# Kernel optimization log

Measured on AMD Instinct MI355X. Metric: run time of the kernel, lower is better.

Reference implementation:

```python
import jax, jax.numpy as jnp
import numpy as np

N, E, D, L = 50000, 640000, 128, 3  # nodes, edges, channels, layers
EPS = 1e-5


def setup_inputs() -> dict:
    key = jax.random.key(0)
    ks = jax.random.split(key, 10)
    s = 1.0 / np.sqrt(D)
    inp = {
        "x": jax.random.normal(ks[0], (N, D), dtype=jnp.float32),
        "edge_attr": jax.random.normal(ks[1], (E, D), dtype=jnp.float32),
        "w_self": jax.random.normal(ks[2], (L, D, D), dtype=jnp.float32) * s,
        "b_self": jnp.zeros((L, D), dtype=jnp.float32),
        "w_in": jax.random.normal(ks[3], (L, D, D), dtype=jnp.float32) * s,
        "b_in": jnp.zeros((L, D), dtype=jnp.float32),
        "w_rel": jax.random.normal(ks[4], (L, D, D), dtype=jnp.float32) * s,
        "b_rel": jnp.zeros((L, D), dtype=jnp.float32),
        "bn_gamma": jnp.ones((L - 1, D), dtype=jnp.float32),
        "bn_beta": jnp.zeros((L - 1, D), dtype=jnp.float32),
        "edge_index": jax.random.randint(ks[5], (2, E), 0, N, dtype=jnp.int64),
    }
    return inp


def _batchnorm(h, gamma, beta):
    mu = jnp.mean(h, axis=0)
    var = jnp.mean(jnp.square(h - mu), axis=0)  # biased var (torch BN training)
    return (h - mu) * jax.lax.rsqrt(var + EPS) * gamma + beta


def reference(x, edge_attr, w_self, b_self, w_in, b_in, w_rel, b_rel,
              bn_gamma, bn_beta, edge_index):
    src, dst = edge_index[0], edge_index[1]
    # per-node in-degree for mean aggregation (zero-degree nodes -> 0)
    cnt = jax.ops.segment_sum(jnp.ones((E, 1), x.dtype), dst, num_segments=N)
    denom = jnp.maximum(cnt, 1.0)
    for i in range(L):
        # message: lin_in(x_j * edge_attr)
        msg = jnp.einsum('ed,fd->ef', x[src] * edge_attr, w_in[i]) + b_in[i]
        agg = jax.ops.segment_sum(msg, dst, num_segments=N) / denom  # scatter-mean
        x = agg + jnp.einsum('nd,fd->nf', x, w_self[i]) + b_self[i]
        edge_attr = jnp.einsum('ed,fd->ef', edge_attr, w_rel[i]) + b_rel[i]
        if i < L - 1:
            x = jax.nn.relu(_batchnorm(x, bn_gamma[i], bn_beta[i]))
            # dropout p=0.0 -> identity
    return (x, edge_attr)
```

## Files before the change

### kernel.cpp

```cpp
#include <hip/hip_runtime.h>

#define DD 128

typedef __attribute__((ext_vector_type(8))) short bf16x8;
typedef __attribute__((ext_vector_type(4))) short bf16x4;
typedef __attribute__((ext_vector_type(4))) float f32x4;
typedef unsigned short u16;

__device__ __forceinline__ unsigned short f2bf(float f) {
  union { float f; unsigned u; } v; v.f = f;
  unsigned u = v.u;
  return (unsigned short)((u + 0x7FFFu + ((u >> 16) & 1u)) >> 16);
}
__device__ __forceinline__ float bf2f(unsigned short h) {
  union { unsigned u; float f; } v; v.u = ((unsigned)h) << 16; return v.f;
}

__device__ __forceinline__ bf16x8 pack8(f32x4 a, f32x4 b) {
  bf16x8 r;
  r[0] = (short)f2bf(a.x); r[1] = (short)f2bf(a.y);
  r[2] = (short)f2bf(a.z); r[3] = (short)f2bf(a.w);
  r[4] = (short)f2bf(b.x); r[5] = (short)f2bf(b.y);
  r[6] = (short)f2bf(b.z); r[7] = (short)f2bf(b.w);
  return r;
}

__device__ __forceinline__ bool idx_is64(const int* p) {
  return (p[1] | p[3] | p[5] | p[7]) == 0;
}
__device__ __forceinline__ int ld_idx(const int* p, long long i, bool is64) {
  return is64 ? (int)((const long long*)p)[i] : p[i];
}

__global__ void k_count(const int* __restrict__ idx, int* __restrict__ cnt, int E) {
  int e = blockIdx.x * blockDim.x + threadIdx.x;
  if (e >= E) return;
  bool is64 = idx_is64(idx);
  int d = ld_idx(idx, (long long)E + e, is64);
  atomicAdd(&cnt[d], 1);
}

__global__ __launch_bounds__(1024) void k_scan(const int* __restrict__ cnt,
    int* __restrict__ row_start, int* __restrict__ cursor, int N) {
  __shared__ int part[1024];
  int t = threadIdx.x;
  int chunk = (N + 1023) >> 10;
  int lo = t * chunk, hi = lo + chunk; if (hi > N) hi = N; if (lo > N) lo = N;
  int s = 0;
  for (int i = lo; i < hi; ++i) s += cnt[i];
  part[t] = s;
  __syncthreads();
  for (int off = 1; off < 1024; off <<= 1) {
    int v = (t >= off) ? part[t - off] : 0;
    __syncthreads();
    part[t] += v;
    __syncthreads();
  }
  int run = (t == 0) ? 0 : part[t - 1];
  for (int i = lo; i < hi; ++i) {
    row_start[i] = run; cursor[i] = run; run += cnt[i];
  }
  if (t == 1023) row_start[N] = part[1023];
}

__global__ void k_fill(const int* __restrict__ idx, int* __restrict__ cursor,
                       int* __restrict__ edge_of, int* __restrict__ src_csr, int E) {
  int e = blockIdx.x * blockDim.x + threadIdx.x;
  if (e >= E) return;
  bool is64 = idx_is64(idx);
  int s = ld_idx(idx, e, is64);
  int d = ld_idx(idx, (long long)E + e, is64);
  int pos = atomicAdd(&cursor[d], 1);
  edge_of[pos] = e;
  src_csr[pos] = s;
}

__global__ __launch_bounds__(256) void k_agg0(const float* __restrict__ x,
    const float* __restrict__ ea, const int* __restrict__ edge_of,
    const int* __restrict__ src_csr, const int* __restrict__ row_start,
    float* __restrict__ aggm, u16* __restrict__ eaC) {
  int n = blockIdx.x * 4 + (threadIdx.x >> 6);
  int lane = threadIdx.x & 63;
  int esub = lane >> 4, cg = lane & 15;
  int c0 = cg * 8;
  int s0 = row_start[n], s1 = row_start[n + 1];
  int len = s1 - s0;
  float acc[8];
#pragma unroll
  for (int j = 0; j < 8; ++j) acc[j] = 0.f;
  for (int kk = 0; kk < len; kk += 4) {
    int kx = kk + esub;
    bool act = kx < len;
    int k = s0 + (act ? kx : 0);
    int e = edge_of[k];
    int sn = src_csr[k];
    f32x4 e0 = *(const f32x4*)(ea + (size_t)e * DD + c0);
    f32x4 e1 = *(const f32x4*)(ea + (size_t)e * DD + c0 + 4);
    f32x4 x0 = *(const f32x4*)(x + (size_t)sn * DD + c0);
    f32x4 x1 = *(const f32x4*)(x + (size_t)sn * DD + c0 + 4);
    if (act) {
      *(bf16x8*)(eaC + (size_t)k * DD + c0) = pack8(e0, e1);
#pragma unroll
      for (int j = 0; j < 4; ++j) acc[j] += x0[j] * e0[j];
#pragma unroll
      for (int j = 0; j < 4; ++j) acc[4 + j] += x1[j] * e1[j];
    }
  }
  float inv = (len > 0) ? 1.0f / (float)len : 0.0f;
#pragma unroll
  for (int j = 0; j < 8; ++j) {
    float s = acc[j];
    s += __shfl_xor(s, 16);
    s += __shfl_xor(s, 32);
    acc[j] = s * inv;
  }
  if (esub == 0) {
    f32x4 lo, hi;
#pragma unroll
    for (int j = 0; j < 4; ++j) { lo[j] = acc[j]; hi[j] = acc[4 + j]; }
    *(f32x4*)(aggm + (size_t)n * DD + c0) = lo;
    *(f32x4*)(aggm + (size_t)n * DD + c0 + 4) = hi;
  }
}

__global__ __launch_bounds__(256) void k_aggN(const u16* __restrict__ xb,
    const u16* __restrict__ eaC, const int* __restrict__ src_csr,
    const int* __restrict__ row_start, const float* __restrict__ scale,
    const float* __restrict__ shift, float* __restrict__ aggm) {
  int n = blockIdx.x * 4 + (threadIdx.x >> 6);
  int lane = threadIdx.x & 63;
  int esub = lane >> 4, cg = lane & 15;
  int c0 = cg * 8;
  float sc[8], sh[8];
#pragma unroll
  for (int j = 0; j < 8; ++j) { sc[j] = scale[c0 + j]; sh[j] = shift[c0 + j]; }
  int s0 = row_start[n], s1 = row_start[n + 1];
  int len = s1 - s0;
  float acc[8];
#pragma unroll
  for (int j = 0; j < 8; ++j) acc[j] = 0.f;
  for (int kk = 0; kk < len; kk += 4) {
    int kx = kk + esub;
    bool act = kx < len;
    int k = s0 + (act ? kx : 0);
    int sn = src_csr[k];
    bf16x8 ev = *(const bf16x8*)(eaC + (size_t)k * DD + c0);
    bf16x8 xv = *(const bf16x8*)(xb + (size_t)sn * DD + c0);
    if (act) {
#pragma unroll
      for (int j = 0; j < 8; ++j) {
        float xf = fmaxf(bf2f((u16)xv[j]) * sc[j] + sh[j], 0.f);
        acc[j] += xf * bf2f((u16)ev[j]);
      }
    }
  }
  float inv = (len > 0) ? 1.0f / (float)len : 0.0f;
#pragma unroll
  for (int j = 0; j < 8; ++j) {
    float s = acc[j];
    s += __shfl_xor(s, 16);
    s += __shfl_xor(s, 32);
    acc[j] = s * inv;
  }
  if (esub == 0) {
    f32x4 lo, hi;
#pragma unroll
    for (int j = 0; j < 4; ++j) { lo[j] = acc[j]; hi[j] = acc[4 + j]; }
    *(f32x4*)(aggm + (size_t)n * DD + c0) = lo;
    *(f32x4*)(aggm + (size_t)n * DD + c0 + 4) = hi;
  }
}

template <typename TX, bool BN, typename TO, bool STATS>
__global__ __launch_bounds__(256) void k_node(const float* __restrict__ aggm,
    const TX* __restrict__ xc, const float* __restrict__ W_in,
    const float* __restrict__ W_self, const float* __restrict__ b_in,
    const float* __restrict__ b_self, const int* __restrict__ row_start,
    const float* __restrict__ scale, const float* __restrict__ shift,
    TO* __restrict__ xn, float* __restrict__ gsum, float* __restrict__ gssq,
    int ntiles) {
  __shared__ short Wl[DD * 256];
  for (int q = threadIdx.x; q < DD * 256 / 4; q += 256) {
    int off = q * 4;
    int f = off >> 8, k = off & 255;
    f32x4 w = (k < 128) ? *(const f32x4*)(W_in + f * 128 + k)
                        : *(const f32x4*)(W_self + f * 128 + (k - 128));
    unsigned byte = ((unsigned)(f * 512 + k * 2)) ^ (unsigned)((f & 7) << 4);
    bf16x4 s4;
    s4[0] = (short)f2bf(w.x); s4[1] = (short)f2bf(w.y);
    s4[2] = (short)f2bf(w.z); s4[3] = (short)f2bf(w.w);
    *(bf16x4*)((char*)Wl + byte) = s4;
  }
  __syncthreads();
  int wave = threadIdx.x >> 6, lane = threadIdx.x & 63;
  int tile = blockIdx.x * 4 + wave;
  if (tile >= ntiles) return;
  int r = lane & 15, g = lane >> 4;
  int arowi = tile * 16 + r;
  const float* arow = aggm + (size_t)arowi * DD;
  const TX* xrow = xc + (size_t)arowi * DD;
  bf16x8 a[8];
#pragma unroll
  for (int ks = 0; ks < 4; ++ks) {
    const float* p = arow + ks * 32 + g * 8;
    a[ks] = pack8(*(const f32x4*)p, *(const f32x4*)(p + 4));
  }
#pragma unroll
  for (int ks = 0; ks < 4; ++ks) {
    int c0 = ks * 32 + g * 8;
    float v[8];
    if constexpr (sizeof(TX) == 2) {
      bf16x8 raw = *(const bf16x8*)(xrow + c0);
#pragma unroll
      for (int j = 0; j < 8; ++j) v[j] = bf2f((u16)raw[j]);
    } else {
      f32x4 r0 = *(const f32x4*)((const float*)xrow + c0);
      f32x4 r1 = *(const f32x4*)((const float*)xrow + c0 + 4);
#pragma unroll
      for (int j = 0; j < 4; ++j) { v[j] = r0[j]; v[4 + j] = r1[j]; }
    }
    bf16x8 fr;
#pragma unroll
    for (int j = 0; j < 8; ++j) {
      float f = v[j];
      if constexpr (BN) f = fmaxf(f * scale[c0 + j] + shift[c0 + j], 0.f);
      fr[j] = (short)f2bf(f);
    }
    a[4 + ks] = fr;
  }
  f32x4 acc[8];
#pragma unroll
  for (int ct = 0; ct < 8; ++ct) acc[ct] = (f32x4){0.f, 0.f, 0.f, 0.f};
#pragma unroll
  for (int ct = 0; ct < 8; ++ct) {
    int f = ct * 16 + r;
    unsigned base = (unsigned)(f * 512);
    unsigned sw = (unsigned)((f & 7) << 4);
#pragma unroll
    for (int ks = 0; ks < 8; ++ks) {
      unsigned byte = (base + (unsigned)(ks * 64 + g * 16)) ^ sw;
      bf16x8 b = *(const bf16x8*)((const char*)Wl + byte);
      acc[ct] = __builtin_amdgcn_mfma_f32_16x16x32_bf16(a[ks], b, acc[ct], 0, 0, 0);
    }
  }
  int nbase = tile * 16;
  float degmask[4];
#pragma unroll
  for (int j = 0; j < 4; ++j) {
    int nn = nbase + g * 4 + j;
    degmask[j] = (row_start[nn + 1] > row_start[nn]) ? 1.0f : 0.0f;
  }
#pragma unroll
  for (int ct = 0; ct < 8; ++ct) {
    int col = ct * 16 + r;
    float bi = b_in[col], bs = b_self[col];
    float s = 0.f, s2 = 0.f;
#pragma unroll
    for (int j = 0; j < 4; ++j) {
      float v = acc[ct][j] + bs + bi * degmask[j];
      if constexpr (sizeof(TO) == 2) xn[(size_t)(nbase + g * 4 + j) * DD + col] = (TO)f2bf(v);
      else                            xn[(size_t)(nbase + g * 4 + j) * DD + col] = (TO)v;
      s += v; s2 += v * v;
    }
    if constexpr (STATS) {
      s += __shfl_xor(s, 16);  s += __shfl_xor(s, 32);
      s2 += __shfl_xor(s2, 16); s2 += __shfl_xor(s2, 32);
      if (g == 0) { atomicAdd(&gsum[col], s); atomicAdd(&gssq[col], s2); }
    }
  }
}

template <bool SCATTER, typename TO>
__global__ __launch_bounds__(256) void k_rel(const u16* __restrict__ ea_in,
    TO* __restrict__ ea_out, const int* __restrict__ edge_of,
    const float* __restrict__ W, const float* __restrict__ bias, int ntiles) {
  __shared__ short Wl[DD * DD];
  for (int q = threadIdx.x; q < DD * DD / 4; q += 256) {
    int off = q * 4;
    int f = off >> 7, d = off & 127;
    f32x4 w = *(const f32x4*)(W + off);
    unsigned byte = ((unsigned)(f * 256 + d * 2)) ^ (unsigned)((f & 7) << 4);
    bf16x4 s4;
    s4[0] = (short)f2bf(w.x); s4[1] = (short)f2bf(w.y);
    s4[2] = (short)f2bf(w.z); s4[3] = (short)f2bf(w.w);
    *(bf16x4*)((char*)Wl + byte) = s4;
  }
  __syncthreads();
  int wave = threadIdx.x >> 6, lane = threadIdx.x & 63;
  int r = lane & 15, g = lane >> 4;
  for (int tile = blockIdx.x * 4 + wave; tile < ntiles; tile += gridDim.x * 4) {
    const u16* rowp = ea_in + (size_t)(tile * 16 + r) * DD;
    bf16x8 a[4];
#pragma unroll
    for (int ks = 0; ks < 4; ++ks) a[ks] = *(const bf16x8*)(rowp + ks * 32 + g * 8);
    f32x4 acc[8];
#pragma unroll
    for (int ct = 0; ct < 8; ++ct) acc[ct] = (f32x4){0.f, 0.f, 0.f, 0.f};
#pragma unroll
    for (int ct = 0; ct < 8; ++ct) {
      int f = ct * 16 + r;
      unsigned base = (unsigned)(f * 256);
      unsigned sw = (unsigned)((f & 7) << 4);
#pragma unroll
      for (int ks = 0; ks < 4; ++ks) {
        unsigned byte = (base + (unsigned)(ks * 64 + g * 16)) ^ sw;
        bf16x8 b = *(const bf16x8*)((const char*)Wl + byte);
        acc[ct] = __builtin_amdgcn_mfma_f32_16x16x32_bf16(a[ks], b, acc[ct], 0, 0, 0);
      }
    }
    size_t orow[4];
#pragma unroll
    for (int j = 0; j < 4; ++j) {
      int kr = tile * 16 + g * 4 + j;
      orow[j] = SCATTER ? (size_t)edge_of[kr] : (size_t)kr;
    }
#pragma unroll
    for (int ct = 0; ct < 8; ++ct) {
      int col = ct * 16 + r;
      float bv = bias[col];
#pragma unroll
      for (int j = 0; j < 4; ++j) {
        float v = acc[ct][j] + bv;
        if constexpr (sizeof(TO) == 2) ea_out[orow[j] * DD + col] = (TO)f2bf(v);
        else                            ea_out[orow[j] * DD + col] = (TO)v;
      }
    }
  }
}

__global__ void k_bnfin(const float* __restrict__ gsum, const float* __restrict__ gssq,
    const float* __restrict__ gamma, const float* __restrict__ beta,
    float* __restrict__ scale, float* __restrict__ shift, int N) {
  int d = threadIdx.x;
  float mu = gsum[d] / (float)N;
  float var = gssq[d] / (float)N - mu * mu;
  float rs = rsqrtf(var + 1e-5f);
  float sc = rs * gamma[d];
  scale[d] = sc;
  shift[d] = beta[d] - mu * sc;
}

static inline size_t alignup(size_t v, size_t a) { return (v + a - 1) & ~(a - 1); }

extern "C" void kernel_launch(void* const* d_in, const int* in_sizes, int n_in,
                              void* d_out, int out_size, void* d_ws, size_t ws_size,
                              hipStream_t stream) {
  const float* x0     = (const float*)d_in[0];
  const float* ea0    = (const float*)d_in[1];
  const float* w_self = (const float*)d_in[2];
  const float* b_self = (const float*)d_in[3];
  const float* w_in   = (const float*)d_in[4];
  const float* b_in   = (const float*)d_in[5];
  const float* w_rel  = (const float*)d_in[6];
  const float* b_rel  = (const float*)d_in[7];
  const float* gamma  = (const float*)d_in[8];
  const float* beta   = (const float*)d_in[9];
  const int*   idx    = (const int*)d_in[10];

  const int N = in_sizes[0] / DD;
  const int E = in_sizes[1] / DD;

  char* w = (char*)d_ws;
  size_t off = 0;
  int* cnt       = (int*)(w + off); off = alignup(off + (size_t)N * 4, 256);
  int* row_start = (int*)(w + off); off = alignup(off + (size_t)(N + 1) * 4, 256);
  int* cursor    = (int*)(w + off); off = alignup(off + (size_t)N * 4, 256);
  int* edge_of   = (int*)(w + off); off = alignup(off + (size_t)E * 4, 256);
  int* src_csr   = (int*)(w + off); off = alignup(off + (size_t)E * 4, 256);
  float* gstats  = (float*)(w + off); off = alignup(off + 256 * 4, 256);
  float* scale   = (float*)(w + off); off = alignup(off + 128 * 4, 256);
  float* shift   = (float*)(w + off); off = alignup(off + 128 * 4, 256);
  float* aggm    = (float*)(w + off); off = alignup(off + (size_t)N * DD * 4, 256);
  u16*   xb      = (u16*)(w + off);   off = alignup(off + (size_t)N * DD * 2, 256);
  u16*   eaC     = (u16*)(w + off);   off = alignup(off + (size_t)E * DD * 2, 256);
  float* gsum = gstats, *gssq = gstats + 128;
  (void)ws_size; (void)n_in; (void)out_size;

  float* out_x  = (float*)d_out;
  float* out_ea = out_x + (size_t)N * DD;

  (void)hipMemsetAsync(cnt, 0, (size_t)N * 4, stream);
  int ethreads = 256, eblocks = (E + ethreads - 1) / ethreads;
  k_count<<<eblocks, ethreads, 0, stream>>>(idx, cnt, E);
  k_scan<<<1, 1024, 0, stream>>>(cnt, row_start, cursor, N);
  k_fill<<<eblocks, ethreads, 0, stream>>>(idx, cursor, edge_of, src_csr, E);

  const int ntN = N / 16;
  const int ntE = E / 16;
  const int aggBlocks = (N + 3) / 4;
  const int nodeBlocks = (ntN + 3) / 4;
  const int relBlocks = 2048;

  (void)hipMemsetAsync(gstats, 0, 256 * 4, stream);
  k_agg0<<<aggBlocks, 256, 0, stream>>>(x0, ea0, edge_of, src_csr, row_start,
                                        aggm, eaC);
  k_node<float, false, u16, true><<<nodeBlocks, 256, 0, stream>>>(aggm, x0,
      w_in, w_self, b_in, b_self, row_start, scale, shift,
      xb, gsum, gssq, ntN);
  k_rel<false, u16><<<relBlocks, 256, 0, stream>>>(eaC, eaC, edge_of,
      w_rel, b_rel, ntE);
  k_bnfin<<<1, 128, 0, stream>>>(gsum, gssq, gamma, beta, scale, shift, N);

  (void)hipMemsetAsync(gstats, 0, 256 * 4, stream);
  k_aggN<<<aggBlocks, 256, 0, stream>>>(xb, eaC, src_csr, row_start,
                                        scale, shift, aggm);
  k_node<u16, true, u16, true><<<nodeBlocks, 256, 0, stream>>>(aggm, xb,
      w_in + DD * DD, w_self + DD * DD, b_in + DD, b_self + DD,
      row_start, scale, shift, xb, gsum, gssq, ntN);
  k_rel<false, u16><<<relBlocks, 256, 0, stream>>>(eaC, eaC, edge_of,
      w_rel + DD * DD, b_rel + DD, ntE);
  k_bnfin<<<1, 128, 0, stream>>>(gsum, gssq, gamma + DD, beta + DD, scale, shift, N);

  k_aggN<<<aggBlocks, 256, 0, stream>>>(xb, eaC, src_csr, row_start,
                                        scale, shift, aggm);
  k_node<u16, true, float, false><<<nodeBlocks, 256, 0, stream>>>(aggm, xb,
      w_in + 2 * DD * DD, w_self + 2 * DD * DD, b_in + 2 * DD, b_self + 2 * DD,
      row_start, scale, shift, out_x, gsum, gssq, ntN);
  k_rel<true, float><<<relBlocks, 256, 0, stream>>>(eaC, out_ea, edge_of,
      w_rel + 2 * DD * DD, b_rel + 2 * DD, ntE);
}
```

Measured before the change: 1.030 ms.

## Split gather-aggregate into edge-parallel message kernel and CSR segment sum

Replaces the per-node gather-and-accumulate kernels with two steps. An edge-parallel kernel writes per-edge bf16 messages (x_src * edge_attr) to a buffer, and a segmented-sum kernel then reduces them per destination node into a bf16 aggregate. BatchNorm+ReLU moves into a separate apply pass over the node features, and the stats reset is folded into the finalize kernel. k_rel now launches one tile per wave instead of a persistent grid. The aim is better load balance and less uncoalesced gather work, at the cost of writing and re-reading a full E×128 message buffer each layer and extra bf16 rounding of messages and aggregates.

```diff
diff --git a/kernel.cpp b/kernel.cpp
--- a/kernel.cpp
+++ b/kernel.cpp
@@ -15,7 +15,6 @@
 __device__ __forceinline__ float bf2f(unsigned short h) {
   union { unsigned u; float f; } v; v.u = ((unsigned)h) << 16; return v.f;
 }
-
 __device__ __forceinline__ bf16x8 pack8(f32x4 a, f32x4 b) {
   bf16x8 r;
   r[0] = (short)f2bf(a.x); r[1] = (short)f2bf(a.y);
@@ -75,108 +74,132 @@
   src_csr[pos] = s;
 }
 
-__global__ __launch_bounds__(256) void k_agg0(const float* __restrict__ x,
-    const float* __restrict__ ea, const int* __restrict__ edge_of,
-    const int* __restrict__ src_csr, const int* __restrict__ row_start,
-    float* __restrict__ aggm, u16* __restrict__ eaC) {
+template <int MODE>
+__global__ __launch_bounds__(256) void k_msg(
+    const float* __restrict__ x0, const u16* __restrict__ xp,
+    const float* __restrict__ ea0, const u16* __restrict__ eain,
+    u16* __restrict__ m, u16* __restrict__ eaC,
+    const int* __restrict__ edge_of, const int* __restrict__ src_csr, int E) {
+  int i = blockIdx.x * 256 + threadIdx.x;
+  int k = i >> 4, c = i & 15;
+  if (k >= E) return;
+  int sn = src_csr[k];
+  int co = c * 8;
+  bf16x8 mm;
+  if constexpr (MODE == 0) {
+    int e = edge_of[k];
+    const float* ep = ea0 + (size_t)e * DD + co;
+    const float* xq = x0 + (size_t)sn * DD + co;
+    f32x4 e0 = *(const f32x4*)ep, e1 = *(const f32x4*)(ep + 4);
+    f32x4 xv0 = *(const f32x4*)xq, xv1 = *(const f32x4*)(xq + 4);
+    *(bf16x8*)(eaC + (size_t)k * DD + co) = pack8(e0, e1);
+    f32x4 p0 = e0 * xv0, p1 = e1 * xv1;
+    mm = pack8(p0, p1);
+  } else {
+    bf16x8 ev = *(const bf16x8*)(eain + (size_t)k * DD + co);
+    bf16x8 xv = *(const bf16x8*)(xp + (size_t)sn * DD + co);
+#pragma unroll
+    for (int j = 0; j < 8; ++j)
+      mm[j] = (short)f2bf(bf2f((u16)ev[j]) * bf2f((u16)xv[j]));
+  }
+  *(bf16x8*)(m + (size_t)k * DD + co) = mm;
+}
+
+__global__ __launch_bounds__(256) void k_segsum(const u16* __restrict__ m,
+    const int* __restrict__ row_start, u16* __restrict__ agg, int N) {
   int n = blockIdx.x * 4 + (threadIdx.x >> 6);
+  if (n >= N) return;
   int lane = threadIdx.x & 63;
-  int esub = lane >> 4, cg = lane & 15;
-  int c0 = cg * 8;
+  int e4 = lane >> 4, c = lane & 15, co = c * 8;
   int s0 = row_start[n], s1 = row_start[n + 1];
   int len = s1 - s0;
   float acc[8];
 #pragma unroll
   for (int j = 0; j < 8; ++j) acc[j] = 0.f;
-  for (int kk = 0; kk < len; kk += 4) {
-    int kx = kk + esub;
-    bool act = kx < len;
-    int k = s0 + (act ? kx : 0);
-    int e = edge_of[k];
-    int sn = src_csr[k];
-    f32x4 e0 = *(const f32x4*)(ea + (size_t)e * DD + c0);
-    f32x4 e1 = *(const f32x4*)(ea + (size_t)e * DD + c0 + 4);
-    f32x4 x0 = *(const f32x4*)(x + (size_t)sn * DD + c0);
-    f32x4 x1 = *(const f32x4*)(x + (size_t)sn * DD + c0 + 4);
-    if (act) {
-      *(bf16x8*)(eaC + (size_t)k * DD + c0) = pack8(e0, e1);
-#pragma unroll
-      for (int j = 0; j < 4; ++j) acc[j] += x0[j] * e0[j];
-#pragma unroll
-      for (int j = 0; j < 4; ++j) acc[4 + j] += x1[j] * e1[j];
-    }
-  }
-  float inv = (len > 0) ? 1.0f / (float)len : 0.0f;
+  for (int kk = e4; kk < len; kk += 4) {
+    bf16x8 mv = *(const bf16x8*)(m + (size_t)(s0 + kk) * DD + co);
+#pragma unroll
+    for (int j = 0; j < 8; ++j) acc[j] += bf2f((u16)mv[j]);
+  }
 #pragma unroll
   for (int j = 0; j < 8; ++j) {
     float s = acc[j];
     s += __shfl_xor(s, 16);
     s += __shfl_xor(s, 32);
-    acc[j] = s * inv;
-  }
-  if (esub == 0) {
+    acc[j] = s;
+  }
+  if (e4 == 0) {
+    float inv = (len > 0) ? 1.0f / (float)len : 0.0f;
     f32x4 lo, hi;
 #pragma unroll
-    for (int j = 0; j < 4; ++j) { lo[j] = acc[j]; hi[j] = acc[4 + j]; }
-    *(f32x4*)(aggm + (size_t)n * DD + c0) = lo;
-    *(f32x4*)(aggm + (size_t)n * DD + c0 + 4) = hi;
-  }
-}
-
-__global__ __launch_bounds__(256) void k_aggN(const u16* __restrict__ xb,
-    const u16* __restrict__ eaC, const int* __restrict__ src_csr,
-    const int* __restrict__ row_start, const float* __restrict__ scale,
-    const float* __restrict__ shift, float* __restrict__ aggm) {
-  int n = blockIdx.x * 4 + (threadIdx.x >> 6);
-  int lane = threadIdx.x & 63;
-  int esub = lane >> 4, cg = lane & 15;
-  int c0 = cg * 8;
-  float sc[8], sh[8];
-#pragma unroll
-  for (int j = 0; j < 8; ++j) { sc[j] = scale[c0 + j]; sh[j] = shift[c0 + j]; }
-  int s0 = row_start[n], s1 = row_start[n + 1];
-  int len = s1 - s0;
-  float acc[8];
-#pragma unroll
-  for (int j = 0; j < 8; ++j) acc[j] = 0.f;
-  for (int kk = 0; kk < len; kk += 4) {
-    int kx = kk + esub;
-    bool act = kx < len;
-    int k = s0 + (act ? kx : 0);
-    int sn = src_csr[k];
-    bf16x8 ev = *(const bf16x8*)(eaC + (size_t)k * DD + c0);
-    bf16x8 xv = *(const bf16x8*)(xb + (size_t)sn * DD + c0);
-    if (act) {
-#pragma unroll
-      for (int j = 0; j < 8; ++j) {
-        float xf = fmaxf(bf2f((u16)xv[j]) * sc[j] + sh[j], 0.f);
-        acc[j] += xf * bf2f((u16)ev[j]);
-      }
-    }
-  }
-  float inv = (len > 0) ? 1.0f / (float)len : 0.0f;
-#pragma unroll
-  for (int j = 0; j < 8; ++j) {
-    float s = acc[j];
-    s += __shfl_xor(s, 16);
-    s += __shfl_xor(s, 32);
-    acc[j] = s * inv;
-  }
-  if (esub == 0) {
-    f32x4 lo, hi;
-#pragma unroll
-    for (int j = 0; j < 4; ++j) { lo[j] = acc[j]; hi[j] = acc[4 + j]; }
-    *(f32x4*)(aggm + (size_t)n * DD + c0) = lo;
-    *(f32x4*)(aggm + (size_t)n * DD + c0 + 4) = hi;
-  }
-}
-
-template <typename TX, bool BN, typename TO, bool STATS>
-__global__ __launch_bounds__(256) void k_node(const float* __restrict__ aggm,
+    for (int j = 0; j < 4; ++j) { lo[j] = acc[j] * inv; hi[j] = acc[4 + j] * inv; }
+    *(bf16x8*)(agg + (size_t)n * DD + co) = pack8(lo, hi);
+  }
+}
+
+template <bool SCATTER, typename TO>
+__global__ __launch_bounds__(256, 3) void k_rel(const u16* __restrict__ ea_in,
+    TO* __restrict__ ea_out, const int* __restrict__ edge_of,
+    const float* __restrict__ W, const float* __restrict__ bias, int ntiles) {
+  __shared__ short Wl[16384];
+  for (int q = threadIdx.x; q < 4096; q += 256) {
+    int off = q * 4;
+    int f = off >> 7, d = off & 127;
+    f32x4 w = *(const f32x4*)(W + off);
+    unsigned byte = ((unsigned)(f * 256 + d * 2)) ^ (unsigned)((f & 7) << 4);
+    bf16x4 s4;
+    s4[0] = (short)f2bf(w.x); s4[1] = (short)f2bf(w.y);
+    s4[2] = (short)f2bf(w.z); s4[3] = (short)f2bf(w.w);
+    *(bf16x4*)((char*)Wl + byte) = s4;
+  }
+  __syncthreads();
+  int wave = threadIdx.x >> 6, lane = threadIdx.x & 63;
+  int r = lane & 15, g = lane >> 4;
+  int tile = blockIdx.x * 4 + wave;
+  if (tile >= ntiles) return;
+  const u16* rowp = ea_in + (size_t)(tile * 16 + r) * DD;
+  bf16x8 a8[4];
+#pragma unroll
+  for (int ks = 0; ks < 4; ++ks) a8[ks] = *(const bf16x8*)(rowp + ks * 32 + g * 8);
+  f32x4 acc[8];
+#pragma unroll
+  for (int ct = 0; ct < 8; ++ct) acc[ct] = (f32x4){0.f, 0.f, 0.f, 0.f};
+#pragma unroll
+  for (int ct = 0; ct < 8; ++ct) {
+    int f = ct * 16 + r;
+    unsigned base = (unsigned)(f * 256);
+    unsigned sw = (unsigned)((f & 7) << 4);
+#pragma unroll
+    for (int ks = 0; ks < 4; ++ks) {
+      unsigned byte = (base + (unsigned)(ks * 64 + g * 16)) ^ sw;
+      bf16x8 bb = *(const bf16x8*)((const char*)Wl + byte);
+      acc[ct] = __builtin_amdgcn_mfma_f32_16x16x32_bf16(a8[ks], bb, acc[ct], 0, 0, 0);
+    }
+  }
+  size_t orow[4];
+#pragma unroll
+  for (int j = 0; j < 4; ++j) {
+    int kr = tile * 16 + g * 4 + j;
+    orow[j] = SCATTER ? (size_t)edge_of[kr] : (size_t)kr;
+  }
+#pragma unroll
+  for (int ct = 0; ct < 8; ++ct) {
+    int col = ct * 16 + r;
+    float bv = bias[col];
+#pragma unroll
+    for (int j = 0; j < 4; ++j) {
+      float v = acc[ct][j] + bv;
+      if constexpr (sizeof(TO) == 2) ea_out[orow[j] * DD + col] = (TO)f2bf(v);
+      else                            ea_out[orow[j] * DD + col] = (TO)v;
+    }
+  }
+}
+
+template <typename TX, typename TO, bool STATS>
+__global__ __launch_bounds__(256, 2) void k_node(const u16* __restrict__ agg,
     const TX* __restrict__ xc, const float* __restrict__ W_in,
     const float* __restrict__ W_self, const float* __restrict__ b_in,
     const float* __restrict__ b_self, const int* __restrict__ row_start,
-    const float* __restrict__ scale, const float* __restrict__ shift,
     TO* __restrict__ xn, float* __restrict__ gsum, float* __restrict__ gssq,
     int ntiles) {
   __shared__ short Wl[DD * 256];
@@ -197,36 +220,20 @@
   if (tile >= ntiles) return;
   int r = lane & 15, g = lane >> 4;
   int arowi = tile * 16 + r;
-  const float* arow = aggm + (size_t)arowi * DD;
+  const u16* arow = agg + (size_t)arowi * DD;
   const TX* xrow = xc + (size_t)arowi * DD;
   bf16x8 a[8];
 #pragma unroll
-  for (int ks = 0; ks < 4; ++ks) {
-    const float* p = arow + ks * 32 + g * 8;
-    a[ks] = pack8(*(const f32x4*)p, *(const f32x4*)(p + 4));
-  }
+  for (int ks = 0; ks < 4; ++ks) a[ks] = *(const bf16x8*)(arow + ks * 32 + g * 8);
 #pragma unroll
   for (int ks = 0; ks < 4; ++ks) {
     int c0 = ks * 32 + g * 8;
-    float v[8];
     if constexpr (sizeof(TX) == 2) {
-      bf16x8 raw = *(const bf16x8*)(xrow + c0);
-#pragma unroll
-      for (int j = 0; j < 8; ++j) v[j] = bf2f((u16)raw[j]);
+      a[4 + ks] = *(const bf16x8*)(xrow + c0);
     } else {
-      f32x4 r0 = *(const f32x4*)((const float*)xrow + c0);
-      f32x4 r1 = *(const f32x4*)((const float*)xrow + c0 + 4);
-#pragma unroll
-      for (int j = 0; j < 4; ++j) { v[j] = r0[j]; v[4 + j] = r1[j]; }
-    }
-    bf16x8 fr;
-#pragma unroll
-    for (int j = 0; j < 8; ++j) {
-      float f = v[j];
-      if constexpr (BN) f = fmaxf(f * scale[c0 + j] + shift[c0 + j], 0.f);
-      fr[j] = (short)f2bf(f);
-    }
-    a[4 + ks] = fr;
+      const float* p = (const float*)xrow + c0;
+      a[4 + ks] = pack8(*(const f32x4*)p, *(const f32x4*)(p + 4));
+    }
   }
   f32x4 acc[8];
 #pragma unroll
@@ -270,65 +277,7 @@
   }
 }
 
-template <bool SCATTER, typename TO>
-__global__ __launch_bounds__(256) void k_rel(const u16* __restrict__ ea_in,
-    TO* __restrict__ ea_out, const int* __restrict__ edge_of,
-    const float* __restrict__ W, const float* __restrict__ bias, int ntiles) {
-  __shared__ short Wl[DD * DD];
-  for (int q = threadIdx.x; q < DD * DD / 4; q += 256) {
-    int off = q * 4;
-    int f = off >> 7, d = off & 127;
-    f32x4 w = *(const f32x4*)(W + off);
-    unsigned byte = ((unsigned)(f * 256 + d * 2)) ^ (unsigned)((f & 7) << 4);
-    bf16x4 s4;
-    s4[0] = (short)f2bf(w.x); s4[1] = (short)f2bf(w.y);
-    s4[2] = (short)f2bf(w.z); s4[3] = (short)f2bf(w.w);
-    *(bf16x4*)((char*)Wl + byte) = s4;
-  }
-  __syncthreads();
-  int wave = threadIdx.x >> 6, lane = threadIdx.x & 63;
-  int r = lane & 15, g = lane >> 4;
-  for (int tile = blockIdx.x * 4 + wave; tile < ntiles; tile += gridDim.x * 4) {
-    const u16* rowp = ea_in + (size_t)(tile * 16 + r) * DD;
-    bf16x8 a[4];
-#pragma unroll
-    for (int ks = 0; ks < 4; ++ks) a[ks] = *(const bf16x8*)(rowp + ks * 32 + g * 8);
-    f32x4 acc[8];
-#pragma unroll
-    for (int ct = 0; ct < 8; ++ct) acc[ct] = (f32x4){0.f, 0.f, 0.f, 0.f};
-#pragma unroll
-    for (int ct = 0; ct < 8; ++ct) {
-      int f = ct * 16 + r;
-      unsigned base = (unsigned)(f * 256);
-      unsigned sw = (unsigned)((f & 7) << 4);
-#pragma unroll
-      for (int ks = 0; ks < 4; ++ks) {
-        unsigned byte = (base + (unsigned)(ks * 64 + g * 16)) ^ sw;
-        bf16x8 b = *(const bf16x8*)((const char*)Wl + byte);
-        acc[ct] = __builtin_amdgcn_mfma_f32_16x16x32_bf16(a[ks], b, acc[ct], 0, 0, 0);
-      }
-    }
-    size_t orow[4];
-#pragma unroll
-    for (int j = 0; j < 4; ++j) {
-      int kr = tile * 16 + g * 4 + j;
-      orow[j] = SCATTER ? (size_t)edge_of[kr] : (size_t)kr;
-    }
-#pragma unroll
-    for (int ct = 0; ct < 8; ++ct) {
-      int col = ct * 16 + r;
-      float bv = bias[col];
-#pragma unroll
-      for (int j = 0; j < 4; ++j) {
-        float v = acc[ct][j] + bv;
-        if constexpr (sizeof(TO) == 2) ea_out[orow[j] * DD + col] = (TO)f2bf(v);
-        else                            ea_out[orow[j] * DD + col] = (TO)v;
-      }
-    }
-  }
-}
-
-__global__ void k_bnfin(const float* __restrict__ gsum, const float* __restrict__ gssq,
+__global__ void k_bnfin(float* __restrict__ gsum, float* __restrict__ gssq,
     const float* __restrict__ gamma, const float* __restrict__ beta,
     float* __restrict__ scale, float* __restrict__ shift, int N) {
   int d = threadIdx.x;
@@ -338,6 +287,24 @@
   float sc = rs * gamma[d];
   scale[d] = sc;
   shift[d] = beta[d] - mu * sc;
+  gsum[d] = 0.f;
+  gssq[d] = 0.f;
+}
+
+__global__ void k_bnapply(const u16* __restrict__ xb, u16* __restrict__ xpost,
+                          const float* __restrict__ scale,
+                          const float* __restrict__ shift, int total8) {
+  int i = blockIdx.x * blockDim.x + threadIdx.x;
+  if (i >= total8) return;
+  bf16x8 v = ((const bf16x8*)xb)[i];
+  int c0 = (i * 8) & 127;
+  bf16x8 o;
+#pragma unroll
+  for (int j = 0; j < 8; ++j) {
+    float f = fmaxf(bf2f((u16)v[j]) * scale[c0 + j] + shift[c0 + j], 0.f);
+    o[j] = (short)f2bf(f);
+  }
+  ((bf16x8*)xpost)[i] = o;
 }
 
 static inline size_t alignup(size_t v, size_t a) { return (v + a - 1) & ~(a - 1); }
@@ -370,9 +337,11 @@
   float* gstats  = (float*)(w + off); off = alignup(off + 256 * 4, 256);
   float* scale   = (float*)(w + off); off = alignup(off + 128 * 4, 256);
   float* shift   = (float*)(w + off); off = alignup(off + 128 * 4, 256);
-  float* aggm    = (float*)(w + off); off = alignup(off + (size_t)N * DD * 4, 256);
-  u16*   xb      = (u16*)(w + off);   off = alignup(off + (size_t)N * DD * 2, 256);
-  u16*   eaC     = (u16*)(w + off);   off = alignup(off + (size_t)E * DD * 2, 256);
+  u16* agg       = (u16*)(w + off); off = alignup(off + (size_t)N * DD * 2, 256);
+  u16* xbA       = (u16*)(w + off); off = alignup(off + (size_t)N * DD * 2, 256);
+  u16* xpost     = (u16*)(w + off); off = alignup(off + (size_t)N * DD * 2, 256);
+  u16* eaC       = (u16*)(w + off); off = alignup(off + (size_t)E * DD * 2, 256);
+  u16* mbuf      = (u16*)(w + off); off = alignup(off + (size_t)E * DD * 2, 256);
   float* gsum = gstats, *gssq = gstats + 128;
   (void)ws_size; (void)n_in; (void)out_size;
 
@@ -384,38 +353,43 @@
   k_count<<<eblocks, ethreads, 0, stream>>>(idx, cnt, E);
   k_scan<<<1, 1024, 0, stream>>>(cnt, row_start, cursor, N);
   k_fill<<<eblocks, ethreads, 0, stream>>>(idx, cursor, edge_of, src_csr, E);
+  (void)hipMemsetAsync(gstats, 0, 256 * 4, stream);
 
   const int ntN = N / 16;
   const int ntE = E / 16;
-  const int aggBlocks = (N + 3) / 4;
+  const int msgBlocks = (E * 16 + 255) / 256;
+  const int segBlocks = (N + 3) / 4;
+  const int relBlocks = (ntE + 3) / 4;
   const int nodeBlocks = (ntN + 3) / 4;
-  const int relBlocks = 2048;
-
-  (void)hipMemsetAsync(gstats, 0, 256 * 4, stream);
-  k_agg0<<<aggBlocks, 256, 0, stream>>>(x0, ea0, edge_of, src_csr, row_start,
-                                        aggm, eaC);
-  k_node<float, false, u16, true><<<nodeBlocks, 256, 0, stream>>>(aggm, x0,
-      w_in, w_self, b_in, b_self, row_start, scale, shift,
-      xb, gsum, gssq, ntN);
+  const int bnBlocks = ((size_t)N * DD / 8 + 255) / 256;
+
+  k_msg<0><<<msgBlocks, 256, 0, stream>>>(x0, nullptr, ea0, nullptr,
+      mbuf, eaC, edge_of, src_csr, E);
   k_rel<false, u16><<<relBlocks, 256, 0, stream>>>(eaC, eaC, edge_of,
       w_rel, b_rel, ntE);
+  k_segsum<<<segBlocks, 256, 0, stream>>>(mbuf, row_start, agg, N);
+  k_node<float, u16, true><<<nodeBlocks, 256, 0, stream>>>(agg, x0,
+      w_in, w_self, b_in, b_self, row_start, xbA, gsum, gssq, ntN);
   k_bnfin<<<1, 128, 0, stream>>>(gsum, gssq, gamma, beta, scale, shift, N);
-
-  (void)hipMemsetAsync(gstats, 0, 256 * 4, stream);
-  k_aggN<<<aggBlocks, 256, 0, stream>>>(xb, eaC, src_csr, row_start,
-                                        scale, shift, aggm);
-  k_node<u16, true, u16, true><<<nodeBlocks, 256, 0, stream>>>(aggm, xb,
-      w_in + DD * DD, w_self + DD * DD, b_in + DD, b_self + DD,
-      row_start, scale, shift, xb, gsum, gssq, ntN);
+  k_bnapply<<<bnBlocks, 256, 0, stream>>>(xbA, xpost, scale, shift, N * DD / 8);
+
+  k_msg<1><<<msgBlocks, 256, 0, stream>>>(nullptr, xpost, nullptr, eaC,
+      mbuf, nullptr, edge_of, src_csr, E);
   k_rel<false, u16><<<relBlocks, 256, 0, stream>>>(eaC, eaC, edge_of,
       w_rel + DD * DD, b_rel + DD, ntE);
+  k_segsum<<<segBlocks, 256, 0, stream>>>(mbuf, row_start, agg, N);
+  k_node<u16, u16, true><<<nodeBlocks, 256, 0, stream>>>(agg, xpost,
+      w_in + DD * DD, w_self + DD * DD, b_in + DD, b_self + DD,
+      row_start, xbA, gsum, gssq, ntN);
   k_bnfin<<<1, 128, 0, stream>>>(gsum, gssq, gamma + DD, beta + DD, scale, shift, N);
-
-  k_aggN<<<aggBlocks, 256, 0, stream>>>(xb, eaC, src_csr, row_start,
-                                        scale, shift, aggm);
-  k_node<u16, true, float, false><<<nodeBlocks, 256, 0, stream>>>(aggm, xb,
-      w_in + 2 * DD * DD, w_self + 2 * DD * DD, b_in + 2 * DD, b_self + 2 * DD,
-      row_start, scale, shift, out_x, gsum, gssq, ntN);
+  k_bnapply<<<bnBlocks, 256, 0, stream>>>(xbA, xpost, scale, shift, N * DD / 8);
+
+  k_msg<1><<<msgBlocks, 256, 0, stream>>>(nullptr, xpost, nullptr, eaC,
+      mbuf, nullptr, edge_of, src_csr, E);
   k_rel<true, float><<<relBlocks, 256, 0, stream>>>(eaC, out_ea, edge_of,
       w_rel + 2 * DD * DD, b_rel + 2 * DD, ntE);
-}
+  k_segsum<<<segBlocks, 256, 0, stream>>>(mbuf, row_start, agg, N);
+  k_node<u16, float, false><<<nodeBlocks, 256, 0, stream>>>(agg, xpost,
+      w_in + 2 * DD * DD, w_self + 2 * DD * DD, b_in + 2 * DD, b_self + 2 * DD,
+      row_start, out_x, gsum, gssq, ntN);
+}
```

Result: slower. 1.215 ms (+18.0%).
